# Optimization experiments

Hardware: AMD Instinct MI355X
Metric: run time of the kernel (lower is better)

Reference implementation:

```python
import math
import jax, jax.numpy as jnp
import numpy as np

B, T, HID = 8, 2048, 1536
H, D = 8, 192
CHUNK, PAST, FUT = 12, 12, 0
CTX = CHUNK + PAST + FUT          # 24
F = PAST + FUT + 1                # 13 relative positions
CAP = 50.0
INVALID = -1.0e9


def setup_inputs() -> dict:
    key = jax.random.key(0)
    k1, k2, k3 = jax.random.split(key, 3)
    x = jax.random.normal(k1, (B, T, HID), dtype=jnp.float32)
    mask = jnp.zeros((B, T), dtype=bool)  # True = invalid/padding
    # causal validity: key offset (c - PAST) relative to query w must lie in [-PAST, FUT]
    w = jnp.arange(CHUNK)[:, None]
    c = jnp.arange(CTX)[None, :]
    causal_valid_mask = (c >= w) & (c <= w + PAST + FUT)  # [CHUNK, CTX]
    W_qkv = jax.random.normal(k2, (HID, 3 * HID), dtype=jnp.float32) * 0.02
    W_pos = jax.random.normal(k3, (HID, HID), dtype=jnp.float32) * 0.02
    per_dim_scale = jnp.zeros((D,), dtype=jnp.float32)
    return {"x": x, "mask": mask, "causal_valid_mask": causal_valid_mask,
            "W_qkv": W_qkv, "W_pos": W_pos, "per_dim_scale": per_dim_scale}


def _extract_block_context(z, U):
    # pad time dim left=PAST, right=FUT+CHUNK-1, then frame with step CHUNK, len CTX
    pad = ((0, 0), (PAST, FUT + CHUNK - 1)) + ((0, 0),) * (z.ndim - 2)
    zp = jnp.pad(z, pad)
    idx = jnp.arange(U)[:, None] * CHUNK + jnp.arange(CTX)[None, :]  # [U, CTX]
    return zp[:, idx]  # [B, U, CTX, ...]


def reference(x, mask, causal_valid_mask, W_qkv, W_pos, per_dim_scale):
    b, t, _ = x.shape
    qkv = x @ W_qkv
    q, k, v = jnp.split(qkv, 3, axis=-1)
    q = q.reshape(b, t, H, D)
    k = k.reshape(b, t, H, D)
    v = v.reshape(b, t, H, D)

    q_scale = D ** (-0.5) / math.log(2.0)
    k_scale = math.log(1.0 + math.e) / math.log(2.0)
    q = q * q_scale * jax.nn.softplus(per_dim_scale)  # per-dim scale on queries
    k = k * k_scale

    U = -(-t // CHUNK)  # ceil
    pad_q = U * CHUNK - t
    qb = jnp.pad(q, ((0, 0), (0, pad_q), (0, 0), (0, 0))).reshape(b, U, CHUNK, H, D)
    kb = _extract_block_context(k, U)            # [B,U,CTX,H,D]
    vb = _extract_block_context(v, U)            # [B,U,CTX,H,D]
    valid = _extract_block_context(~mask, U)     # [B,U,CTX]

    # ---- relative position embedding (Transformer-XL style) ----
    pos = jnp.arange(PAST, -FUT - 1, -1, dtype=jnp.float32)  # [F]
    nts = HID // 2
    inv_ts = jnp.exp(jnp.arange(nts, dtype=jnp.float32) * (-(math.log(10000.0) / (nts - 1))))
    st = pos[:, None] * inv_ts[None, :]
    emb = jnp.concatenate([jnp.sin(st), jnp.cos(st)], axis=-1)  # [F, HID]
    sin_emb = (emb @ W_pos).reshape(F, H, D)

    term_ac = jnp.einsum('buwhd,buchd->bhuwc', qb, kb)     # content-content
    term_bd = jnp.einsum('buwhd,fhd->bhuwf', qb, sin_emb)  # content-position
    # relative shift: pad last dim to CTX+1, flatten, slice, reshape
    pad_amt = CTX + 1 - F
    tb = jnp.pad(term_bd, ((0, 0),) * 4 + ((0, pad_amt),))
    tb = tb.reshape(b, H, U, CHUNK * (CTX + 1))[..., :CHUNK * CTX]
    tb = tb.reshape(b, H, U, CHUNK, CTX)

    logits = term_ac + tb
    logits = jnp.tanh(logits / CAP) * CAP  # softcap
    cond = valid[:, None, :, None, :] & causal_valid_mask[None, None, None, :, :]
    logits = jnp.where(cond, logits, INVALID)
    probs = jax.nn.softmax(logits, axis=-1)
    out = jnp.einsum('bhuwc,buchd->buwhd', probs, vb)
    return out.reshape(b, U * CHUNK, H, D)[:, :t]
```

## Files before the change

kernel.cpp:

```cpp
#include <hip/hip_runtime.h>

typedef unsigned int u32;
typedef unsigned short u16;

typedef __attribute__((ext_vector_type(8))) short bf16x8;
typedef __attribute__((ext_vector_type(4))) float f32x4;

__device__ __forceinline__ u16 f2bf(float f) {
  u32 u = __builtin_bit_cast(u32, f);
  u32 r = (u + 0x7fffu + ((u >> 16) & 1u)) >> 16;
  return (u16)r;
}
__device__ __forceinline__ float bfl(u32 u) { return __builtin_bit_cast(float, u << 16); }
__device__ __forceinline__ float bfh(u32 u) { return __builtin_bit_cast(float, u & 0xffff0000u); }

__device__ __forceinline__ void gload_lds16(const u16* g, u16* l) {
  __builtin_amdgcn_global_load_lds(
      (const __attribute__((address_space(1))) void*)g,
      (__attribute__((address_space(3))) void*)l, 16, 0, 0);
}

__global__ __launch_bounds__(256) void transp_wt(const float* __restrict__ W,
                                                 u16* __restrict__ Wt) {
  __shared__ float tile[64][68];
  int bk = blockIdx.x % 24, bn = blockIdx.x / 24;
  int k0 = bk * 64, n0 = bn * 64;
  int tid = threadIdx.x;
#pragma unroll
  for (int p = 0; p < 4; p++) {
    int idx = p * 256 + tid;
    int r = idx >> 4, c4 = idx & 15;
    *(float4*)&tile[r][c4 * 4] = *(const float4*)&W[(size_t)(k0 + r) * 4608 + n0 + c4 * 4];
  }
  __syncthreads();
#pragma unroll
  for (int p = 0; p < 2; p++) {
    int idx = p * 256 + tid;
    int rn = idx >> 3, kc = idx & 7;
    u16 pk[8];
#pragma unroll
    for (int e = 0; e < 8; e++) pk[e] = f2bf(tile[kc * 8 + e][rn]);
    *(uint4*)&Wt[(size_t)(n0 + rn) * 1536 + k0 + kc * 8] = *(const uint4*)pk;
  }
}

__global__ __launch_bounds__(256) void conv_x(const float* __restrict__ X,
                                              u16* __restrict__ Xb) {
  int i = blockIdx.x * 256 + threadIdx.x;
  const float4* xp = (const float4*)X;
  float4 a = xp[i * 2], b = xp[i * 2 + 1];
  uint4 o;
  o.x = (u32)f2bf(a.x) | ((u32)f2bf(a.y) << 16);
  o.y = (u32)f2bf(a.z) | ((u32)f2bf(a.w) << 16);
  o.z = (u32)f2bf(b.x) | ((u32)f2bf(b.y) << 16);
  o.w = (u32)f2bf(b.z) | ((u32)f2bf(b.w) << 16);
  ((uint4*)Xb)[i] = o;
}

__global__ __launch_bounds__(256) void pos_emb_part(const float* __restrict__ Wp,
                                                    float* __restrict__ part) {
  __shared__ float er[13 * 32];
  int ks = blockIdx.x % 48, nb = blockIdx.x / 48;
  int tid = threadIdx.x;
  int n = nb * 256 + tid;
  const float cfreq = 9.210340371976184f / 767.0f;
  for (int i = tid; i < 13 * 32; i += 256) {
    int f = i >> 5, kk = i & 31;
    int k = ks * 32 + kk;
    int ii = (k < 768) ? k : (k - 768);
    float fr = expf(-cfreq * (float)ii);
    float st = (float)(12 - f) * fr;
    er[f * 32 + kk] = (k < 768) ? sinf(st) : cosf(st);
  }
  __syncthreads();
  float acc[13];
#pragma unroll
  for (int f = 0; f < 13; f++) acc[f] = 0.f;
  const float* wp = Wp + (size_t)(ks * 32) * 1536 + n;
  for (int kk = 0; kk < 32; kk++) {
    float w = wp[(size_t)kk * 1536];
#pragma unroll
    for (int f = 0; f < 13; f++) acc[f] = fmaf(er[f * 32 + kk], w, acc[f]);
  }
#pragma unroll
  for (int f = 0; f < 13; f++)
    part[((size_t)ks * 13 + f) * 1536 + n] = acc[f];
}

__global__ __launch_bounds__(256) void pos_emb_red(const float* __restrict__ part,
                                                   u16* __restrict__ sembbf) {
  int idxg = blockIdx.x * 256 + threadIdx.x;
  int f = idxg / 1536, n = idxg % 1536;
  float s = 0.f;
  if (f < 13)
    for (int ks = 0; ks < 48; ks++)
      s += part[((size_t)ks * 13 + f) * 1536 + n];
  sembbf[idxg] = f2bf(s);
}

__global__ __launch_bounds__(512, 4) void gemm_qkv(const u16* __restrict__ Xb,
                                                   const u16* __restrict__ Bt,
                                                   u16* __restrict__ C,
                                                   const float* __restrict__ pds) {
  extern __shared__ u16 smem[];

  const int tid = threadIdx.x;
  const int lane = tid & 63;
  const int wv = tid >> 6;
  const int wr = wv >> 2;
  const int wc = wv & 3;
  const int lr = lane & 15;
  const int lkq = lane >> 4;
  const int sx = lr & 7;

  int bid = blockIdx.x;
  int xcd = bid & 7, idx = bid >> 3;
  int bm = xcd * 16 + idx / 24;
  int bn = idx % 24;
  int m0 = bm * 128, n0 = bn * 192;

  auto stageA = [&](int T) {
#pragma unroll
    for (int q = 0; q < 2; q++) {
      int ch = q * 512 + tid;
      int r = ch >> 3, cr = ch & 7;
      int crs = cr ^ (r & 7);
      const u16* g = Xb + (size_t)(m0 + r) * 1536 + T * 64 + crs * 8;
      u16* l = smem + (T & 1) * 8192 + ch * 8;
      gload_lds16(g, l);
    }
  };
  auto stageB = [&](int T) {
#pragma unroll
    for (int q = 0; q < 3; q++) {
      int ch = q * 512 + tid;
      int r = ch >> 3, cr = ch & 7;
      int crs = cr ^ (r & 7);
      const u16* g = Bt + (size_t)(n0 + r) * 1536 + T * 64 + crs * 8;
      u16* l = smem + 16384 + (T & 1) * 12288 + ch * 8;
      gload_lds16(g, l);
    }
  };

  f32x4 acc[4][3];
#pragma unroll
  for (int i = 0; i < 4; i++)
#pragma unroll
    for (int j = 0; j < 3; j++) acc[i][j] = (f32x4){0.f, 0.f, 0.f, 0.f};

  stageA(0); stageB(0);
  asm volatile("s_waitcnt vmcnt(0)" ::: "memory");
  __builtin_amdgcn_s_barrier();

  bf16x8 af[8], bfr[6];

  for (int t = 0; t < 24; t++) {
    const int ab = (t & 1) * 8192;
    const int bb = 16384 + (t & 1) * 12288;

    if (t < 23) { stageA(t + 1); stageB(t + 1); }

#pragma unroll
    for (int j = 0; j < 3; j++)
#pragma unroll
      for (int ks = 0; ks < 2; ks++) {
        int R = wc * 48 + j * 16 + lr;
        bfr[j * 2 + ks] = *(const bf16x8*)&smem[bb + R * 64 + ((ks * 4 + lkq) ^ sx) * 8];
      }
#pragma unroll
    for (int i = 0; i < 4; i++)
#pragma unroll
      for (int ks = 0; ks < 2; ks++) {
        int R = wr * 64 + i * 16 + lr;
        af[i * 2 + ks] = *(const bf16x8*)&smem[ab + R * 64 + ((ks * 4 + lkq) ^ sx) * 8];
      }

    __builtin_amdgcn_s_setprio(1);
#pragma unroll
    for (int i = 0; i < 4; i++)
#pragma unroll
      for (int j = 0; j < 3; j++)
#pragma unroll
        for (int ks = 0; ks < 2; ks++)
          acc[i][j] = __builtin_amdgcn_mfma_f32_16x16x32_bf16(af[i * 2 + ks], bfr[j * 2 + ks], acc[i][j], 0, 0, 0);
    __builtin_amdgcn_s_setprio(0);

    asm volatile("s_waitcnt vmcnt(0)" ::: "memory");
    __builtin_amdgcn_s_barrier();
  }

  const float kscale = 1.8946361f;
  float scl[3];
#pragma unroll
  for (int j = 0; j < 3; j++) {
    int gcol = n0 + wc * 48 + j * 16 + lr;
    float s;
    if (gcol < 1536) s = 0.10411754f * log1pf(expf(pds[gcol % 192]));
    else if (gcol < 3072) s = kscale;
    else s = 1.0f;
    scl[j] = s;
  }
  int r0 = lkq * 4;
#pragma unroll
  for (int i = 0; i < 4; i++)
#pragma unroll
    for (int j = 0; j < 3; j++) {
      int row = wr * 64 + i * 16 + r0;
      int col = wc * 48 + j * 16 + lr;
#pragma unroll
      for (int r = 0; r < 4; r++)
        smem[(row + r) * 200 + col] = f2bf(acc[i][j][r] * scl[j]);
    }
  asm volatile("s_waitcnt lgkmcnt(0)" ::: "memory");
  __builtin_amdgcn_s_barrier();
#pragma unroll
  for (int p = 0; p < 6; p++) {
    int idx2 = p * 512 + tid;
    int row = idx2 / 24, cq = idx2 % 24;
    *(uint4*)&C[(size_t)(m0 + row) * 4608 + n0 + cq * 8] =
        *(const uint4*)&smem[row * 200 + cq * 8];
  }
}

__global__ __launch_bounds__(512) void qsemb(const u16* __restrict__ qkv,
                                             const u16* __restrict__ sembbf,
                                             float* __restrict__ bdall) {
  int tid = threadIdx.x;
  int lane = tid & 63;
  int h = tid >> 6;
  int t0 = blockIdx.x * 16;
  int arow = lane & 15, ak = lane >> 4;

  const u16* qp = qkv + (size_t)(t0 + arow) * 4608 + h * 192 + ak * 8;
  const u16* sp = sembbf + (size_t)(lane & 15) * 1536 + h * 192 + ak * 8;

  f32x4 acc = (f32x4){0.f, 0.f, 0.f, 0.f};
#pragma unroll
  for (int kt = 0; kt < 6; kt++) {
    bf16x8 a = *(const bf16x8*)(qp + kt * 32);
    bf16x8 bb = *(const bf16x8*)(sp + kt * 32);
    acc = __builtin_amdgcn_mfma_f32_16x16x32_bf16(a, bb, acc, 0, 0, 0);
  }
  int f = lane & 15;
  int rbase = (lane >> 4) * 4;
  if (f < 13) {
#pragma unroll
    for (int r = 0; r < 4; r++)
      bdall[(size_t)(t0 + rbase + r) * 104 + h * 13 + f] = acc[r];
  }
}

__global__ __launch_bounds__(256) void attn_kernel(const u16* __restrict__ qkv,
                                                   const float* __restrict__ bdall,
                                                   const unsigned char* __restrict__ mask,
                                                   float* __restrict__ out) {
  __shared__ u16 sq[24 * 200];
  __shared__ u16 sk[36 * 200];
  __shared__ u16 sv[36 * 200];
  __shared__ float lg[24 * 14];
  __shared__ int vld[36];

  int bid = blockIdx.x;
  int h = bid & 7;
  int u2 = (bid >> 3) % 86;
  int b = bid / (86 * 8);
  int tid = threadIdx.x;
  int tbase = u2 * 24;

  if (tid < 36) {
    int t = tbase + tid - 12;
    vld[tid] = (t >= 0 && t < 2048 && mask[b * 2048 + t] == 0) ? 1 : 0;
  }

  const u16* base = qkv + (size_t)b * 2048 * 4608 + h * 192;
  for (int idx = tid; idx < 576; idx += 256) {
    int w = idx / 24, g = idx % 24;
    int t = tbase + w;
    uint4 val = {0u, 0u, 0u, 0u};
    if (t < 2048) val = *(const uint4*)(base + (size_t)t * 4608 + g * 8);
    *(uint4*)&sq[w * 200 + g * 8] = val;
  }
  for (int idx = tid; idx < 1728; idx += 256) {
    int kv = idx / 864, r = idx % 864;
    int c = r / 24, g = r % 24;
    int t = tbase + c - 12;
    uint4 val = {0u, 0u, 0u, 0u};
    if (t >= 0 && t < 2048)
      val = *(const uint4*)(base + (size_t)t * 4608 + (kv ? 3072 : 1536) + g * 8);
    if (kv) *(uint4*)&sv[c * 200 + g * 8] = val;
    else    *(uint4*)&sk[c * 200 + g * 8] = val;
  }
  __syncthreads();

  for (int idx = tid; idx < 312; idx += 256) {
    int w = idx % 24, f = idx / 24;
    int c = w + f;
    int t = tbase + w;
    float l = -1e9f;
    if (vld[c] && t < 2048) {
      float ac = 0.f;
      const u16* qp = &sq[w * 200];
      const u16* kp = &sk[c * 200];
#pragma unroll 4
      for (int i = 0; i < 24; i++) {
        uint4 qa = *(const uint4*)(qp + i * 8);
        uint4 kb = *(const uint4*)(kp + i * 8);
        ac = fmaf(bfl(qa.x), bfl(kb.x), ac);
        ac = fmaf(bfh(qa.x), bfh(kb.x), ac);
        ac = fmaf(bfl(qa.y), bfl(kb.y), ac);
        ac = fmaf(bfh(qa.y), bfh(kb.y), ac);
        ac = fmaf(bfl(qa.z), bfl(kb.z), ac);
        ac = fmaf(bfh(qa.z), bfh(kb.z), ac);
        ac = fmaf(bfl(qa.w), bfl(kb.w), ac);
        ac = fmaf(bfh(qa.w), bfh(kb.w), ac);
      }
      float bd = bdall[(size_t)(b * 2048 + t) * 104 + h * 13 + f];
      l = tanhf((ac + bd) * 0.02f) * 50.f;
    }
    lg[w * 14 + f] = l;
  }
  __syncthreads();

  if (tid < 24) {
    float m = -3e38f;
#pragma unroll
    for (int f = 0; f < 13; f++) m = fmaxf(m, lg[tid * 14 + f]);
    float s = 0.f;
#pragma unroll
    for (int f = 0; f < 13; f++) {
      float e = expf(lg[tid * 14 + f] - m);
      lg[tid * 14 + f] = e;
      s += e;
    }
    float inv = 1.f / s;
#pragma unroll
    for (int f = 0; f < 13; f++) lg[tid * 14 + f] *= inv;
  }
  __syncthreads();

  for (int idx = tid; idx < 1152; idx += 256) {
    int w = idx / 48, g = idx % 48;
    int t = tbase + w;
    if (t >= 2048) continue;
    float a0 = 0, a1 = 0, a2 = 0, a3 = 0;
#pragma unroll
    for (int f = 0; f < 13; f++) {
      float p = lg[w * 14 + f];
      uint2 vv = *(const uint2*)&sv[(w + f) * 200 + g * 4];
      a0 = fmaf(p, bfl(vv.x), a0);
      a1 = fmaf(p, bfh(vv.x), a1);
      a2 = fmaf(p, bfl(vv.y), a2);
      a3 = fmaf(p, bfh(vv.y), a3);
    }
    float4 o = {a0, a1, a2, a3};
    *(float4*)&out[(((size_t)(b * 2048 + t)) * 8 + h) * 192 + g * 4] = o;
  }
}

extern "C" void kernel_launch(void* const* d_in, const int* in_sizes, int n_in,
                              void* d_out, int out_size, void* d_ws, size_t ws_size,
                              hipStream_t stream) {
  (void)in_sizes; (void)n_in; (void)out_size; (void)ws_size;
  const float* x = (const float*)d_in[0];
  const unsigned char* mask = (const unsigned char*)d_in[1];
  const float* Wqkv = (const float*)d_in[3];
  const float* Wpos = (const float*)d_in[4];
  const float* pds = (const float*)d_in[5];
  float* out = (float*)d_out;

  char* ws = (char*)d_ws;
  u16* Wt = (u16*)ws;
  u16* qkv = (u16*)(ws + 14155776);
  u16* Xb = (u16*)(ws + 165150720);
  u16* sembbf = (u16*)(ws + 215482368);
  float* bdall = (float*)(ws + 215531520);
  float* part = (float*)(ws + 222347264);

  transp_wt<<<1728, 256, 0, stream>>>(Wqkv, Wt);
  conv_x<<<12288, 256, 0, stream>>>(x, Xb);
  pos_emb_part<<<288, 256, 0, stream>>>(Wpos, part);
  pos_emb_red<<<96, 256, 0, stream>>>(part, sembbf);
  gemm_qkv<<<3072, 512, 81920, stream>>>(Xb, Wt, qkv, pds);
  qsemb<<<1024, 512, 0, stream>>>(qkv, sembbf, bdall);
  attn_kernel<<<5504, 256, 0, stream>>>(qkv, bdall, mask, out);
}
```

Measured before the change: 380.8 us.

## Enlarge QKV GEMM block tile to 512x192 with per-wave 128x96 tiles

The QKV GEMM block tile grows from 128x192 to 512x192, with each of the 8 waves computing a 128x96 sub-tile of 48 accumulators. The K step shrinks from 64 to 32, so the LDS swizzle changes to a 4-chunk XOR. The epilogue now writes the output in two halves through the staging buffer. The goal is to raise the MFMA-to-LDS-read ratio and cut redundant loads of the B matrix. The cost is a much higher register footprint (occupancy bound relaxed to 2), fewer blocks (768), more loop iterations with barriers, and a serialized epilogue.

```diff
diff --git a/kernel.cpp b/kernel.cpp
--- a/kernel.cpp
+++ b/kernel.cpp
@@ -98,7 +98,7 @@
   sembbf[idxg] = f2bf(s);
 }
 
-__global__ __launch_bounds__(512, 4) void gemm_qkv(const u16* __restrict__ Xb,
+__global__ __launch_bounds__(512, 2) void gemm_qkv(const u16* __restrict__ Xb,
                                                    const u16* __restrict__ Bt,
                                                    u16* __restrict__ C,
                                                    const float* __restrict__ pds) {
@@ -107,82 +107,80 @@
   const int tid = threadIdx.x;
   const int lane = tid & 63;
   const int wv = tid >> 6;
-  const int wr = wv >> 2;
-  const int wc = wv & 3;
+  const int wr = wv >> 1;
+  const int wc = wv & 1;
   const int lr = lane & 15;
   const int lkq = lane >> 4;
-  const int sx = lr & 7;
+  const int sx = (lr >> 2) & 3;
 
   int bid = blockIdx.x;
   int xcd = bid & 7, idx = bid >> 3;
-  int bm = xcd * 16 + idx / 24;
+  int bm = xcd * 4 + idx / 24;
   int bn = idx % 24;
-  int m0 = bm * 128, n0 = bn * 192;
+  int m0 = bm * 512, n0 = bn * 192;
 
   auto stageA = [&](int T) {
 #pragma unroll
-    for (int q = 0; q < 2; q++) {
+    for (int q = 0; q < 4; q++) {
       int ch = q * 512 + tid;
-      int r = ch >> 3, cr = ch & 7;
-      int crs = cr ^ (r & 7);
-      const u16* g = Xb + (size_t)(m0 + r) * 1536 + T * 64 + crs * 8;
-      u16* l = smem + (T & 1) * 8192 + ch * 8;
+      int r = ch >> 2, cp = ch & 3;
+      int gc = cp ^ ((r >> 2) & 3);
+      const u16* g = Xb + (size_t)(m0 + r) * 1536 + T * 32 + gc * 8;
+      u16* l = smem + (T & 1) * 16384 + ch * 8;
       gload_lds16(g, l);
     }
   };
   auto stageB = [&](int T) {
-#pragma unroll
-    for (int q = 0; q < 3; q++) {
-      int ch = q * 512 + tid;
-      int r = ch >> 3, cr = ch & 7;
-      int crs = cr ^ (r & 7);
-      const u16* g = Bt + (size_t)(n0 + r) * 1536 + T * 64 + crs * 8;
-      u16* l = smem + 16384 + (T & 1) * 12288 + ch * 8;
-      gload_lds16(g, l);
+    {
+      int ch = tid;
+      int r = ch >> 2, cp = ch & 3;
+      int gc = cp ^ ((r >> 2) & 3);
+      gload_lds16(Bt + (size_t)(n0 + r) * 1536 + T * 32 + gc * 8,
+                  smem + 32768 + (T & 1) * 6144 + ch * 8);
+    }
+    if (tid < 256) {
+      int ch = 512 + tid;
+      int r = ch >> 2, cp = ch & 3;
+      int gc = cp ^ ((r >> 2) & 3);
+      gload_lds16(Bt + (size_t)(n0 + r) * 1536 + T * 32 + gc * 8,
+                  smem + 32768 + (T & 1) * 6144 + ch * 8);
     }
   };
 
-  f32x4 acc[4][3];
-#pragma unroll
-  for (int i = 0; i < 4; i++)
-#pragma unroll
-    for (int j = 0; j < 3; j++) acc[i][j] = (f32x4){0.f, 0.f, 0.f, 0.f};
+  f32x4 acc[8][6];
+#pragma unroll
+  for (int i = 0; i < 8; i++)
+#pragma unroll
+    for (int j = 0; j < 6; j++) acc[i][j] = (f32x4){0.f, 0.f, 0.f, 0.f};
 
   stageA(0); stageB(0);
   asm volatile("s_waitcnt vmcnt(0)" ::: "memory");
   __builtin_amdgcn_s_barrier();
 
-  bf16x8 af[8], bfr[6];
-
-  for (int t = 0; t < 24; t++) {
-    const int ab = (t & 1) * 8192;
-    const int bb = 16384 + (t & 1) * 12288;
-
-    if (t < 23) { stageA(t + 1); stageB(t + 1); }
-
-#pragma unroll
-    for (int j = 0; j < 3; j++)
-#pragma unroll
-      for (int ks = 0; ks < 2; ks++) {
-        int R = wc * 48 + j * 16 + lr;
-        bfr[j * 2 + ks] = *(const bf16x8*)&smem[bb + R * 64 + ((ks * 4 + lkq) ^ sx) * 8];
-      }
-#pragma unroll
-    for (int i = 0; i < 4; i++)
-#pragma unroll
-      for (int ks = 0; ks < 2; ks++) {
-        int R = wr * 64 + i * 16 + lr;
-        af[i * 2 + ks] = *(const bf16x8*)&smem[ab + R * 64 + ((ks * 4 + lkq) ^ sx) * 8];
-      }
+  for (int t = 0; t < 48; t++) {
+    const int ab = (t & 1) * 16384;
+    const int bb = 32768 + (t & 1) * 6144;
+
+    if (t < 47) { stageA(t + 1); stageB(t + 1); }
+
+    bf16x8 af[8], bfr[6];
+#pragma unroll
+    for (int i = 0; i < 8; i++) {
+      int R = wr * 128 + i * 16 + lr;
+      af[i] = *(const bf16x8*)&smem[ab + R * 32 + (lkq ^ sx) * 8];
+    }
+#pragma unroll
+    for (int j = 0; j < 6; j++) {
+      int R = wc * 96 + j * 16 + lr;
+      bfr[j] = *(const bf16x8*)&smem[bb + R * 32 + (lkq ^ sx) * 8];
+    }
 
     __builtin_amdgcn_s_setprio(1);
 #pragma unroll
-    for (int i = 0; i < 4; i++)
-#pragma unroll
-      for (int j = 0; j < 3; j++)
-#pragma unroll
-        for (int ks = 0; ks < 2; ks++)
-          acc[i][j] = __builtin_amdgcn_mfma_f32_16x16x32_bf16(af[i * 2 + ks], bfr[j * 2 + ks], acc[i][j], 0, 0, 0);
+    for (int i = 0; i < 8; i++)
+#pragma unroll
+      for (int j = 0; j < 6; j++)
+        acc[i][j] = __builtin_amdgcn_mfma_f32_16x16x32_bf16(af[i], bfr[j], acc[i][j], 0, 0, 0);
     __builtin_amdgcn_s_setprio(0);
 
     asm volatile("s_waitcnt vmcnt(0)" ::: "memory");
@@ -190,35 +188,41 @@
   }
 
   const float kscale = 1.8946361f;
-  float scl[3];
-#pragma unroll
-  for (int j = 0; j < 3; j++) {
-    int gcol = n0 + wc * 48 + j * 16 + lr;
+  float scl[6];
+#pragma unroll
+  for (int j = 0; j < 6; j++) {
+    int gcol = n0 + wc * 96 + j * 16 + lr;
     float s;
     if (gcol < 1536) s = 0.10411754f * log1pf(expf(pds[gcol % 192]));
     else if (gcol < 3072) s = kscale;
     else s = 1.0f;
     scl[j] = s;
   }
-  int r0 = lkq * 4;
-#pragma unroll
-  for (int i = 0; i < 4; i++)
-#pragma unroll
-    for (int j = 0; j < 3; j++) {
-      int row = wr * 64 + i * 16 + r0;
-      int col = wc * 48 + j * 16 + lr;
-#pragma unroll
-      for (int r = 0; r < 4; r++)
-        smem[(row + r) * 200 + col] = f2bf(acc[i][j][r] * scl[j]);
-    }
-  asm volatile("s_waitcnt lgkmcnt(0)" ::: "memory");
-  __builtin_amdgcn_s_barrier();
-#pragma unroll
-  for (int p = 0; p < 6; p++) {
-    int idx2 = p * 512 + tid;
-    int row = idx2 / 24, cq = idx2 % 24;
-    *(uint4*)&C[(size_t)(m0 + row) * 4608 + n0 + cq * 8] =
-        *(const uint4*)&smem[row * 200 + cq * 8];
+#pragma unroll
+  for (int h = 0; h < 2; h++) {
+    if ((wr >> 1) == h) {
+      int rb = (wr & 1) * 128;
+#pragma unroll
+      for (int i = 0; i < 8; i++)
+#pragma unroll
+        for (int j = 0; j < 6; j++) {
+          int row = rb + i * 16 + lkq * 4;
+          int col = wc * 96 + j * 16 + lr;
+#pragma unroll
+          for (int r = 0; r < 4; r++)
+            smem[(row + r) * 200 + col] = f2bf(acc[i][j][r] * scl[j]);
+        }
+    }
+    asm volatile("s_waitcnt lgkmcnt(0)" ::: "memory");
+    __builtin_amdgcn_s_barrier();
+#pragma unroll
+    for (int p = 0; p < 12; p++) {
+      int idx2 = p * 512 + tid;
+      int row = idx2 / 24, cq = idx2 % 24;
+      *(uint4*)&C[(size_t)(m0 + h * 256 + row) * 4608 + n0 + cq * 8] =
+          *(const uint4*)&smem[row * 200 + cq * 8];
+    }
+    __builtin_amdgcn_s_barrier();
   }
 }
 
@@ -380,7 +384,7 @@
   conv_x<<<12288, 256, 0, stream>>>(x, Xb);
   pos_emb_part<<<288, 256, 0, stream>>>(Wpos, part);
   pos_emb_red<<<96, 256, 0, stream>>>(part, sembbf);
-  gemm_qkv<<<3072, 512, 81920, stream>>>(Xb, Wt, qkv, pds);
+  gemm_qkv<<<768, 512, 102400, stream>>>(Xb, Wt, qkv, pds);
   qsemb<<<1024, 512, 0, stream>>>(qkv, sembbf, bdall);
   attn_kernel<<<5504, 256, 0, stream>>>(qkv, bdall, mask, out);
 }
```

Result: slower. 489.9 us (+28.7%).
